# Performance work log

Measured on AMD Instinct MI355X. Metric: run time of the kernel, lower is better.

The kernel has to match this reference:

```python
import jax, jax.numpy as jnp
import numpy as np

N, E, G = 20000, 320000, 64   # nodes, edges, graphs in batch
DIN, DH, H, C = 128, 64, 8, 32  # in dim, hidden per head, heads, classes
NEG_SLOPE = 0.2


def setup_inputs() -> dict:
    key = jax.random.key(0)
    ks = jax.random.split(key, 20)
    s = lambda fan: 1.0 / np.sqrt(fan)
    inp = {
        "g_feats": jax.random.normal(ks[0], (N, DIN), jnp.float32),
        "src": jax.random.randint(ks[1], (E,), 0, N),
        "dst": jax.random.randint(ks[2], (E,), 0, N),
        "graph_ids": jnp.sort(jax.random.randint(ks[3], (N,), 0, G)),
        # input layer (linear): dim_in -> dim_h
        "W_in": jax.random.normal(ks[4], (DIN, DH), jnp.float32) * s(DIN),
        "b_in": jnp.zeros((DH,), jnp.float32),
        # GATv2 layer 1: dim_h -> H * dim_h
        "Wsrc1": jax.random.normal(ks[5], (DH, H * DH), jnp.float32) * s(DH),
        "bsrc1": jnp.zeros((H * DH,), jnp.float32),
        "Wdst1": jax.random.normal(ks[6], (DH, H * DH), jnp.float32) * s(DH),
        "bdst1": jnp.zeros((H * DH,), jnp.float32),
        "attn1": jax.random.normal(ks[7], (H, DH), jnp.float32) * s(DH),
        "bias1": jnp.zeros((H * DH,), jnp.float32),
        # GATv2 layer 2
        "Wsrc2": jax.random.normal(ks[8], (DH, H * DH), jnp.float32) * s(DH),
        "bsrc2": jnp.zeros((H * DH,), jnp.float32),
        "Wdst2": jax.random.normal(ks[9], (DH, H * DH), jnp.float32) * s(DH),
        "bdst2": jnp.zeros((H * DH,), jnp.float32),
        "attn2": jax.random.normal(ks[10], (H, DH), jnp.float32) * s(DH),
        "bias2": jnp.zeros((H * DH,), jnp.float32),
        # classification head: Linear(DH,DH) -> relu -> Linear(DH,C) -> softmax
        "Wh1": jax.random.normal(ks[11], (DH, DH), jnp.float32) * s(DH),
        "bh1": jnp.zeros((DH,), jnp.float32),
        "Wh2": jax.random.normal(ks[12], (DH, C), jnp.float32) * s(DH),
        "bh2": jnp.zeros((C,), jnp.float32),
    }
    return inp


def gatv2(h, src, dst, Ws, bs, Wd, bd, attn, bias):
    # DGL GATv2Conv: e_uv = attn . leaky_relu(fc_src(h_u) + fc_dst(h_v)),
    # softmax over incoming edges of v, aggregate fc_src(h_u).
    fs = (h @ Ws + bs).reshape(N, H, DH)
    fd = (h @ Wd + bd).reshape(N, H, DH)
    e = jax.nn.leaky_relu(fs[src] + fd[dst], NEG_SLOPE)      # [E, H, DH]
    scores = jnp.einsum('ehd,hd->eh', e, attn)               # [E, H]
    m = jax.ops.segment_max(scores, dst, num_segments=N)     # [N, H]
    m = jnp.where(jnp.isfinite(m), m, 0.0)                   # nodes w/o in-edges
    w = jnp.exp(scores - m[dst])
    denom = jax.ops.segment_sum(w, dst, num_segments=N)
    alpha = w / jnp.maximum(denom[dst], 1e-9)                # [E, H]
    out = jax.ops.segment_sum(fs[src] * alpha[:, :, None], dst, num_segments=N)
    return out + bias.reshape(1, H, DH)                      # [N, H, DH]


def reference(g_feats, src, dst, graph_ids, W_in, b_in,
              Wsrc1, bsrc1, Wdst1, bdst1, attn1, bias1,
              Wsrc2, bsrc2, Wdst2, bdst2, attn2, bias2,
              Wh1, bh1, Wh2, bh2):
    h = g_feats @ W_in + b_in                                # input layer ('linear')
    h = gatv2(h, src, dst, Wsrc1, bsrc1, Wdst1, bdst1, attn1, bias1).mean(axis=1)
    h = jax.nn.relu(h)
    h = gatv2(h, src, dst, Wsrc2, bsrc2, Wdst2, bdst2, attn2, bias2).mean(axis=1)
    # mean readout per graph
    sums = jax.ops.segment_sum(h, graph_ids, num_segments=G)
    counts = jax.ops.segment_sum(jnp.ones((N,), h.dtype), graph_ids, num_segments=G)
    hg = sums / jnp.maximum(counts, 1.0)[:, None]            # [G, DH]
    # head: Linear -> relu -> Linear -> softmax (dropout = identity at eval)
    logits = jax.nn.relu(hg @ Wh1 + bh1) @ Wh2 + bh2
    return jax.nn.softmax(logits, axis=-1)
```

## Files before the change

kernel.cpp:

```cpp
#include <hip/hip_runtime.h>

#define NN 20000
#define NE 320000
#define NG 64
#define DIN 128
#define DH 64
#define NH 8
#define HD 512
#define NC 32

typedef unsigned short ushort_t;
typedef unsigned int uint_t;

__device__ __forceinline__ ushort_t f2bf(float f) {
  uint_t x = __float_as_uint(f);
  uint_t r = (x + 0x7fffu + ((x >> 16) & 1u)) >> 16;
  return (ushort_t)r;
}

template<int PAT>
__device__ __forceinline__ float swz(float v) {
  return __int_as_float(__builtin_amdgcn_ds_swizzle(__float_as_int(v), PAT));
}

__device__ __forceinline__ void gemm_in_tile(const float* __restrict__ gf,
    const float* __restrict__ W_in, const float* __restrict__ b_in,
    float* __restrict__ h0, int tile) {
  __shared__ float AsIn[16][DIN];
  const int t = threadIdx.x;
  const int row0 = tile * 16;
  for (int i = t; i < 16 * DIN; i += 256)
    AsIn[i >> 7][i & 127] = gf[(size_t)(row0 + (i >> 7)) * DIN + (i & 127)];
  __syncthreads();
  const int c = t & 63, rg = t >> 6;
  float acc[4] = {0.f, 0.f, 0.f, 0.f};
  for (int k = 0; k < DIN; ++k) {
    float w = W_in[k * DH + c];
#pragma unroll
    for (int i = 0; i < 4; ++i) acc[i] += AsIn[rg * 4 + i][k] * w;
  }
  float b = b_in[c];
#pragma unroll
  for (int i = 0; i < 4; ++i)
    h0[(size_t)(row0 + rg * 4 + i) * DH + c] = acc[i] + b;
}

__device__ __forceinline__ void pair_tile(const float* __restrict__ A,
    const float* __restrict__ Ws, const float* __restrict__ bs,
    const float* __restrict__ Wd, const float* __restrict__ bd,
    ushort_t* __restrict__ fsb, float* __restrict__ fd, int tile) {
  __shared__ float AsP[16][DH];
  const int t = threadIdx.x;
  const bool isFd = tile >= (NN / 16);
  const int bx = isFd ? tile - (NN / 16) : tile;
  const float* W = isFd ? Wd : Ws;
  const float* b = isFd ? bd : bs;
  const int row0 = bx * 16;
  {
    int idx = t * 4;
    int r = idx >> 6, k = idx & 63;
    *(float4*)&AsP[r][k] = *(const float4*)&A[(size_t)(row0 + r) * DH + k];
  }
  __syncthreads();
  const int tc = t & 127;
  const int tr = t >> 7;
  float acc[8][4];
#pragma unroll
  for (int r = 0; r < 8; ++r)
#pragma unroll
    for (int c = 0; c < 4; ++c) acc[r][c] = 0.f;
#pragma unroll 4
  for (int k = 0; k < DH; ++k) {
    float4 wv = *(const float4*)&W[k * HD + 4 * tc];
#pragma unroll
    for (int r = 0; r < 8; ++r) {
      float a = AsP[tr * 8 + r][k];
      acc[r][0] += a * wv.x; acc[r][1] += a * wv.y;
      acc[r][2] += a * wv.z; acc[r][3] += a * wv.w;
    }
  }
  float4 bv = *(const float4*)&b[4 * tc];
#pragma unroll
  for (int r = 0; r < 8; ++r) {
    int row = row0 + tr * 8 + r;
    float v0 = acc[r][0] + bv.x, v1 = acc[r][1] + bv.y;
    float v2 = acc[r][2] + bv.z, v3 = acc[r][3] + bv.w;
    if (!isFd) {
      ushort4 o;
      o.x = f2bf(v0); o.y = f2bf(v1); o.z = f2bf(v2); o.w = f2bf(v3);
      *(ushort4*)&fsb[(size_t)row * HD + 4 * tc] = o;
    } else {
      *(float4*)&fd[(size_t)row * HD + 4 * tc] = make_float4(v0, v1, v2, v3);
    }
  }
}

__global__ __launch_bounds__(256) void k_pre(const float* __restrict__ gf,
    const float* __restrict__ W_in, const float* __restrict__ b_in,
    float* __restrict__ h0, const int* __restrict__ dst, int* __restrict__ counts,
    const int* __restrict__ gid, int* __restrict__ gs) {
  const int bid = blockIdx.x;
  if (bid < NN / 16) {
    gemm_in_tile(gf, W_in, b_in, h0, bid);
  } else if (bid < NN / 16 + NE / 256) {
    int e = (bid - NN / 16) * 256 + threadIdx.x;
    atomicAdd(&counts[dst[e]], 1);
  } else {
    int i = (bid - (NN / 16 + NE / 256)) * 256 + threadIdx.x;
    if (i > NN) return;
    if (i == 0) {
      for (int g = 0; g <= gid[0]; ++g) gs[g] = 0;
    } else if (i == NN) {
      for (int g = gid[NN - 1] + 1; g <= NG; ++g) gs[g] = NN;
    } else {
      int a = gid[i - 1], b2 = gid[i];
      for (int g = a + 1; g <= b2; ++g) gs[g] = i;
    }
  }
}

__global__ __launch_bounds__(256) void k_assign(const int* __restrict__ counts,
    int* __restrict__ row_beg, int* __restrict__ row_end, int* __restrict__ cursor,
    int* __restrict__ gcounter) {
  const int i = blockIdx.x * 256 + threadIdx.x;
  const int lane = threadIdx.x & 63;
  int cnt = (i < NN) ? counts[i] : 0;
  int pre = cnt;
#pragma unroll
  for (int d = 1; d < 64; d <<= 1) {
    int o = __shfl_up(pre, d);
    if (lane >= d) pre += o;
  }
  int total = __shfl(pre, 63);
  int excl = pre - cnt;
  int base = 0;
  if (lane == 63 && total > 0) base = atomicAdd(gcounter, total);
  base = __shfl(base, 63);
  if (i < NN) {
    int b = base + excl;
    row_beg[i] = b;
    row_end[i] = b + cnt;
    cursor[i] = b;
  }
}

__global__ __launch_bounds__(256) void k_scatpair(const float* __restrict__ A,
    const float* __restrict__ Ws, const float* __restrict__ bs,
    const float* __restrict__ Wd, const float* __restrict__ bd,
    ushort_t* __restrict__ fsb, float* __restrict__ fd,
    const int* __restrict__ dst, const int* __restrict__ src,
    int* __restrict__ cursor, int* __restrict__ src_sorted) {
  const int bid = blockIdx.x;
  if (bid < 2 * (NN / 16)) {
    pair_tile(A, Ws, bs, Wd, bd, fsb, fd, bid);
  } else {
    int e = (bid - 2 * (NN / 16)) * 256 + threadIdx.x;
    int p = atomicAdd(&cursor[dst[e]], 1);
    src_sorted[p] = src[e];
  }
}

__global__ __launch_bounds__(256) void k_pair(const float* __restrict__ A,
    const float* __restrict__ Ws, const float* __restrict__ bs,
    const float* __restrict__ Wd, const float* __restrict__ bd,
    ushort_t* __restrict__ fsb, float* __restrict__ fd) {
  pair_tile(A, Ws, bs, Wd, bd, fsb, fd, blockIdx.x);
}

__global__ __launch_bounds__(256) void k_gat(const ushort_t* __restrict__ fsb,
    const float* __restrict__ fd, const int* __restrict__ src_sorted,
    const int* __restrict__ row_beg, const int* __restrict__ row_end,
    const float* __restrict__ attn, const float* __restrict__ bias,
    float* __restrict__ hout, int do_relu) {
  const int lane = threadIdx.x & 63;
  const int v = blockIdx.x * 4 + (threadIdx.x >> 6);
  const int fi = lane * 8;
  float fdv[8], av[8];
  *(float4*)&fdv[0] = *(const float4*)&fd[(size_t)v * HD + fi];
  *(float4*)&fdv[4] = *(const float4*)&fd[(size_t)v * HD + fi + 4];
  *(float4*)&av[0]  = *(const float4*)&attn[fi];
  *(float4*)&av[4]  = *(const float4*)&attn[fi + 4];
  int e = row_beg[v];
  const int end = row_end[v];
  float m = -3.4e38f, sum = 0.f;
  float acc[8];
#pragma unroll
  for (int i = 0; i < 8; ++i) acc[i] = 0.f;
  for (; e + 1 < end; e += 2) {
    int sA = src_sorted[e], sB = src_sorted[e + 1];
    uint4 uA = *(const uint4*)&fsb[(size_t)sA * HD + fi];
    uint4 uB = *(const uint4*)&fsb[(size_t)sB * HD + fi];
    float fA[8], fB[8];
    fA[0] = __uint_as_float(uA.x << 16); fA[1] = __uint_as_float(uA.x & 0xffff0000u);
    fA[2] = __uint_as_float(uA.y << 16); fA[3] = __uint_as_float(uA.y & 0xffff0000u);
    fA[4] = __uint_as_float(uA.z << 16); fA[5] = __uint_as_float(uA.z & 0xffff0000u);
    fA[6] = __uint_as_float(uA.w << 16); fA[7] = __uint_as_float(uA.w & 0xffff0000u);
    fB[0] = __uint_as_float(uB.x << 16); fB[1] = __uint_as_float(uB.x & 0xffff0000u);
    fB[2] = __uint_as_float(uB.y << 16); fB[3] = __uint_as_float(uB.y & 0xffff0000u);
    fB[4] = __uint_as_float(uB.z << 16); fB[5] = __uint_as_float(uB.z & 0xffff0000u);
    fB[6] = __uint_as_float(uB.w << 16); fB[7] = __uint_as_float(uB.w & 0xffff0000u);
    float pA = 0.f, pB = 0.f;
#pragma unroll
    for (int i = 0; i < 8; ++i) {
      float xA = fA[i] + fdv[i];
      float lA = fmaxf(xA, 0.f) + 0.2f * fminf(xA, 0.f);
      pA = fmaf(av[i], lA, pA);
      float xB = fB[i] + fdv[i];
      float lB = fmaxf(xB, 0.f) + 0.2f * fminf(xB, 0.f);
      pB = fmaf(av[i], lB, pB);
    }
    pA += swz<0x041F>(pA); pB += swz<0x041F>(pB);
    pA += swz<0x081F>(pA); pB += swz<0x081F>(pB);
    pA += swz<0x101F>(pA); pB += swz<0x101F>(pB);
    float mn = fmaxf(m, fmaxf(pA, pB));
    float scale = __expf(m - mn);
    float wA = __expf(pA - mn), wB = __expf(pB - mn);
    sum = fmaf(sum, scale, wA + wB);
#pragma unroll
    for (int i = 0; i < 8; ++i)
      acc[i] = fmaf(acc[i], scale, fmaf(wA, fA[i], wB * fB[i]));
    m = mn;
  }
  if (e < end) {
    int sA = src_sorted[e];
    uint4 uA = *(const uint4*)&fsb[(size_t)sA * HD + fi];
    float fA[8];
    fA[0] = __uint_as_float(uA.x << 16); fA[1] = __uint_as_float(uA.x & 0xffff0000u);
    fA[2] = __uint_as_float(uA.y << 16); fA[3] = __uint_as_float(uA.y & 0xffff0000u);
    fA[4] = __uint_as_float(uA.z << 16); fA[5] = __uint_as_float(uA.z & 0xffff0000u);
    fA[6] = __uint_as_float(uA.w << 16); fA[7] = __uint_as_float(uA.w & 0xffff0000u);
    float pA = 0.f;
#pragma unroll
    for (int i = 0; i < 8; ++i) {
      float xA = fA[i] + fdv[i];
      float lA = fmaxf(xA, 0.f) + 0.2f * fminf(xA, 0.f);
      pA = fmaf(av[i], lA, pA);
    }
    pA += swz<0x041F>(pA);
    pA += swz<0x081F>(pA);
    pA += swz<0x101F>(pA);
    float mn = fmaxf(m, pA);
    float scale = __expf(m - mn);
    float wA = __expf(pA - mn);
    sum = fmaf(sum, scale, wA);
#pragma unroll
    for (int i = 0; i < 8; ++i)
      acc[i] = fmaf(acc[i], scale, wA * fA[i]);
  }
  float inv = 1.f / fmaxf(sum, 1e-9f);
  float outv[8];
#pragma unroll
  for (int i = 0; i < 8; ++i) outv[i] = fmaf(acc[i], inv, bias[fi + i]);
#pragma unroll
  for (int i = 0; i < 8; ++i) {
    outv[i] += swz<0x201F>(outv[i]);
    outv[i] += swz<0x401F>(outv[i]);
    outv[i] += __shfl_xor(outv[i], 32);
    outv[i] *= 0.125f;
    if (do_relu) outv[i] = fmaxf(outv[i], 0.f);
  }
  if (lane < 8) {
    *(float4*)&hout[(size_t)v * DH + lane * 8]     = make_float4(outv[0], outv[1], outv[2], outv[3]);
    *(float4*)&hout[(size_t)v * DH + lane * 8 + 4] = make_float4(outv[4], outv[5], outv[6], outv[7]);
  }
}

__global__ __launch_bounds__(256) void k_head(const float* __restrict__ h2,
    const int* __restrict__ gsv, const float* __restrict__ Wh1,
    const float* __restrict__ bh1, const float* __restrict__ Wh2,
    const float* __restrict__ bh2, float* __restrict__ out) {
  __shared__ float part[4][DH];
  __shared__ float hg[DH];
  __shared__ float hid[DH];
  __shared__ float logits[NC];
  const int g = blockIdx.x;
  const int t = threadIdx.x;
  const int f = t & 63, chunk = t >> 6;
  int start = gsv[g], stop = gsv[g + 1];
  float s = 0.f;
  for (int r = start + chunk; r < stop; r += 4) s += h2[(size_t)r * DH + f];
  part[chunk][f] = s;
  __syncthreads();
  if (t < DH) {
    float tot = part[0][t] + part[1][t] + part[2][t] + part[3][t];
    hg[t] = tot / fmaxf((float)(stop - start), 1.f);
  }
  __syncthreads();
  if (t < DH) {
    float a = 0.f;
    for (int k = 0; k < DH; ++k) a += hg[k] * Wh1[k * DH + t];
    hid[t] = fmaxf(a + bh1[t], 0.f);
  }
  __syncthreads();
  if (t < NC) {
    float l = 0.f;
    for (int k = 0; k < DH; ++k) l += hid[k] * Wh2[k * NC + t];
    logits[t] = l + bh2[t];
  }
  __syncthreads();
  if (t == 0) {
    float mx = logits[0];
    for (int i = 1; i < NC; ++i) mx = fmaxf(mx, logits[i]);
    float sm = 0.f;
    for (int i = 0; i < NC; ++i) {
      float wv = __expf(logits[i] - mx);
      logits[i] = wv;
      sm += wv;
    }
    float inv = 1.f / sm;
    for (int i = 0; i < NC; ++i) out[g * NC + i] = logits[i] * inv;
  }
}

extern "C" void kernel_launch(void* const* d_in, const int* in_sizes, int n_in,
                              void* d_out, int out_size, void* d_ws, size_t ws_size,
                              hipStream_t stream) {
  const float* g_feats = (const float*)d_in[0];
  const int*   src     = (const int*)d_in[1];
  const int*   dst     = (const int*)d_in[2];
  const int*   gid     = (const int*)d_in[3];
  const float* W_in    = (const float*)d_in[4];
  const float* b_in    = (const float*)d_in[5];
  const float* Wsrc1   = (const float*)d_in[6];
  const float* bsrc1   = (const float*)d_in[7];
  const float* Wdst1   = (const float*)d_in[8];
  const float* bdst1   = (const float*)d_in[9];
  const float* attn1   = (const float*)d_in[10];
  const float* bias1   = (const float*)d_in[11];
  const float* Wsrc2   = (const float*)d_in[12];
  const float* bsrc2   = (const float*)d_in[13];
  const float* Wdst2   = (const float*)d_in[14];
  const float* bdst2   = (const float*)d_in[15];
  const float* attn2   = (const float*)d_in[16];
  const float* bias2   = (const float*)d_in[17];
  const float* Wh1     = (const float*)d_in[18];
  const float* bh1     = (const float*)d_in[19];
  const float* Wh2     = (const float*)d_in[20];
  const float* bh2     = (const float*)d_in[21];

  char* ws = (char*)d_ws;
  size_t off = 0;
  auto A = [&](size_t bytes) -> char* {
    char* q = ws + off;
    off = (off + bytes + 255) & ~(size_t)255;
    return q;
  };
  float*    h0         = (float*)A((size_t)NN * DH * 4);
  float*    h1         = (float*)A((size_t)NN * DH * 4);
  float*    h2         = (float*)A((size_t)NN * DH * 4);
  ushort_t* fsb        = (ushort_t*)A((size_t)NN * HD * 2);
  float*    fd         = (float*)A((size_t)NN * HD * 4);
  int*      row_beg    = (int*)A((size_t)NN * 4);
  int*      row_end    = (int*)A((size_t)NN * 4);
  int*      cursor     = (int*)A((size_t)NN * 4);
  int*      src_sorted = (int*)A((size_t)NE * 4);
  int*      gs         = (int*)A((size_t)(NG + 1) * 4);
  int*      counts     = (int*)A((size_t)(NN + 1) * 4);

  const int nb16 = NN / 16;
  const int histb = NE / 256;
  const int gbb = (NN + 256) / 256;

  hipMemsetAsync(counts, 0, (size_t)(NN + 1) * 4, stream);

  k_pre<<<nb16 + histb + gbb, 256, 0, stream>>>(g_feats, W_in, b_in, h0,
                                                dst, counts, gid, gs);
  k_assign<<<(NN + 255) / 256, 256, 0, stream>>>(counts, row_beg, row_end,
                                                 cursor, &counts[NN]);
  k_scatpair<<<2 * nb16 + histb, 256, 0, stream>>>(h0, Wsrc1, bsrc1, Wdst1, bdst1,
                                                   fsb, fd, dst, src, cursor, src_sorted);
  k_gat<<<NN / 4, 256, 0, stream>>>(fsb, fd, src_sorted, row_beg, row_end,
                                    attn1, bias1, h1, 1);
  k_pair<<<2 * nb16, 256, 0, stream>>>(h1, Wsrc2, bsrc2, Wdst2, bdst2, fsb, fd);
  k_gat<<<NN / 4, 256, 0, stream>>>(fsb, fd, src_sorted, row_beg, row_end,
                                    attn2, bias2, h2, 0);
  k_head<<<NG, 256, 0, stream>>>(h2, gs, Wh1, bh1, Wh2, bh2, (float*)d_out);
}
```

Measured before the change: 341.8 us.

## Retile projection GEMM to 32 rows x 512 threads and unroll GAT edge loop by four

The fsrc/fdst projection now uses 512-thread blocks. Each thread owns one output column across 32 rows, replacing the previous 16-row tiles with a 4-column-per-thread layout. This halves the block count and reuses each weight load across more rows, but it writes bf16 outputs as scalar 2-byte stores. The GAT aggregation loop now processes four edges per iteration instead of two, exposing more independent gathers for memory-level parallelism at the cost of higher register pressure. The tail is now a loop and correctly updates the running max.

```diff
diff --git a/kernel.cpp b/kernel.cpp
--- a/kernel.cpp
+++ b/kernel.cpp
@@ -45,53 +45,48 @@
     h0[(size_t)(row0 + rg * 4 + i) * DH + c] = acc[i] + b;
 }
 
+#define ROWS_P 32
+#define TPM 625
 __device__ __forceinline__ void pair_tile(const float* __restrict__ A,
     const float* __restrict__ Ws, const float* __restrict__ bs,
     const float* __restrict__ Wd, const float* __restrict__ bd,
     ushort_t* __restrict__ fsb, float* __restrict__ fd, int tile) {
-  __shared__ float AsP[16][DH];
+  __shared__ float4 AsP4[ROWS_P][16];
   const int t = threadIdx.x;
-  const bool isFd = tile >= (NN / 16);
-  const int bx = isFd ? tile - (NN / 16) : tile;
+  const bool isFd = tile >= TPM;
+  const int bx = isFd ? tile - TPM : tile;
   const float* W = isFd ? Wd : Ws;
   const float* b = isFd ? bd : bs;
-  const int row0 = bx * 16;
+  const int row0 = bx * ROWS_P;
   {
-    int idx = t * 4;
-    int r = idx >> 6, k = idx & 63;
-    *(float4*)&AsP[r][k] = *(const float4*)&A[(size_t)(row0 + r) * DH + k];
-  }
-  __syncthreads();
-  const int tc = t & 127;
-  const int tr = t >> 7;
-  float acc[8][4];
-#pragma unroll
-  for (int r = 0; r < 8; ++r)
-#pragma unroll
-    for (int c = 0; c < 4; ++c) acc[r][c] = 0.f;
-#pragma unroll 4
-  for (int k = 0; k < DH; ++k) {
-    float4 wv = *(const float4*)&W[k * HD + 4 * tc];
-#pragma unroll
-    for (int r = 0; r < 8; ++r) {
-      float a = AsP[tr * 8 + r][k];
-      acc[r][0] += a * wv.x; acc[r][1] += a * wv.y;
-      acc[r][2] += a * wv.z; acc[r][3] += a * wv.w;
-    }
-  }
-  float4 bv = *(const float4*)&b[4 * tc];
-#pragma unroll
-  for (int r = 0; r < 8; ++r) {
-    int row = row0 + tr * 8 + r;
-    float v0 = acc[r][0] + bv.x, v1 = acc[r][1] + bv.y;
-    float v2 = acc[r][2] + bv.z, v3 = acc[r][3] + bv.w;
-    if (!isFd) {
-      ushort4 o;
-      o.x = f2bf(v0); o.y = f2bf(v1); o.z = f2bf(v2); o.w = f2bf(v3);
-      *(ushort4*)&fsb[(size_t)row * HD + 4 * tc] = o;
-    } else {
-      *(float4*)&fd[(size_t)row * HD + 4 * tc] = make_float4(v0, v1, v2, v3);
-    }
+    int row = t >> 4, kq = t & 15;
+    AsP4[row][kq] = *(const float4*)&A[(size_t)(row0 + row) * DH + 4 * kq];
+  }
+  __syncthreads();
+  const int c = t;
+  float acc[ROWS_P];
+#pragma unroll
+  for (int r = 0; r < ROWS_P; ++r) acc[r] = 0.f;
+  for (int kb = 0; kb < 16; ++kb) {
+    float w0 = W[(size_t)(4 * kb + 0) * HD + c];
+    float w1 = W[(size_t)(4 * kb + 1) * HD + c];
+    float w2 = W[(size_t)(4 * kb + 2) * HD + c];
+    float w3 = W[(size_t)(4 * kb + 3) * HD + c];
+#pragma unroll
+    for (int r = 0; r < ROWS_P; ++r) {
+      float4 a = AsP4[r][kb];
+      acc[r] = fmaf(a.x, w0, fmaf(a.y, w1, fmaf(a.z, w2, fmaf(a.w, w3, acc[r]))));
+    }
+  }
+  float bv = b[c];
+  if (!isFd) {
+#pragma unroll
+    for (int r = 0; r < ROWS_P; ++r)
+      fsb[(size_t)(row0 + r) * HD + c] = f2bf(acc[r] + bv);
+  } else {
+#pragma unroll
+    for (int r = 0; r < ROWS_P; ++r)
+      fd[(size_t)(row0 + r) * HD + c] = acc[r] + bv;
   }
 }
 
@@ -100,13 +95,14 @@
     float* __restrict__ h0, const int* __restrict__ dst, int* __restrict__ counts,
     const int* __restrict__ gid, int* __restrict__ gs) {
   const int bid = blockIdx.x;
-  if (bid < NN / 16) {
+  const int NB_IN = NN / 16;
+  if (bid < NB_IN) {
     gemm_in_tile(gf, W_in, b_in, h0, bid);
-  } else if (bid < NN / 16 + NE / 256) {
-    int e = (bid - NN / 16) * 256 + threadIdx.x;
+  } else if (bid < NB_IN + NE / 256) {
+    int e = (bid - NB_IN) * 256 + threadIdx.x;
     atomicAdd(&counts[dst[e]], 1);
   } else {
-    int i = (bid - (NN / 16 + NE / 256)) * 256 + threadIdx.x;
+    int i = (bid - (NB_IN + NE / 256)) * 256 + threadIdx.x;
     if (i > NN) return;
     if (i == 0) {
       for (int g = 0; g <= gid[0]; ++g) gs[g] = 0;
@@ -144,23 +140,23 @@
   }
 }
 
-__global__ __launch_bounds__(256) void k_scatpair(const float* __restrict__ A,
+__global__ __launch_bounds__(512) void k_scatpair(const float* __restrict__ A,
     const float* __restrict__ Ws, const float* __restrict__ bs,
     const float* __restrict__ Wd, const float* __restrict__ bd,
     ushort_t* __restrict__ fsb, float* __restrict__ fd,
     const int* __restrict__ dst, const int* __restrict__ src,
     int* __restrict__ cursor, int* __restrict__ src_sorted) {
   const int bid = blockIdx.x;
-  if (bid < 2 * (NN / 16)) {
+  if (bid < 2 * TPM) {
     pair_tile(A, Ws, bs, Wd, bd, fsb, fd, bid);
   } else {
-    int e = (bid - 2 * (NN / 16)) * 256 + threadIdx.x;
+    int e = (bid - 2 * TPM) * 512 + threadIdx.x;
     int p = atomicAdd(&cursor[dst[e]], 1);
     src_sorted[p] = src[e];
   }
 }
 
-__global__ __launch_bounds__(256) void k_pair(const float* __restrict__ A,
+__global__ __launch_bounds__(512) void k_pair(const float* __restrict__ A,
     const float* __restrict__ Ws, const float* __restrict__ bs,
     const float* __restrict__ Wd, const float* __restrict__ bd,
     ushort_t* __restrict__ fsb, float* __restrict__ fd) {
@@ -186,11 +182,14 @@
   float acc[8];
 #pragma unroll
   for (int i = 0; i < 8; ++i) acc[i] = 0.f;
-  for (; e + 1 < end; e += 2) {
-    int sA = src_sorted[e], sB = src_sorted[e + 1];
+  for (; e + 3 < end; e += 4) {
+    int sA = src_sorted[e],     sB = src_sorted[e + 1];
+    int sC = src_sorted[e + 2], sD = src_sorted[e + 3];
     uint4 uA = *(const uint4*)&fsb[(size_t)sA * HD + fi];
     uint4 uB = *(const uint4*)&fsb[(size_t)sB * HD + fi];
-    float fA[8], fB[8];
+    uint4 uC = *(const uint4*)&fsb[(size_t)sC * HD + fi];
+    uint4 uD = *(const uint4*)&fsb[(size_t)sD * HD + fi];
+    float fA[8], fB[8], fC[8], fD[8];
     fA[0] = __uint_as_float(uA.x << 16); fA[1] = __uint_as_float(uA.x & 0xffff0000u);
     fA[2] = __uint_as_float(uA.y << 16); fA[3] = __uint_as_float(uA.y & 0xffff0000u);
     fA[4] = __uint_as_float(uA.z << 16); fA[5] = __uint_as_float(uA.z & 0xffff0000u);
@@ -199,29 +198,41 @@
     fB[2] = __uint_as_float(uB.y << 16); fB[3] = __uint_as_float(uB.y & 0xffff0000u);
     fB[4] = __uint_as_float(uB.z << 16); fB[5] = __uint_as_float(uB.z & 0xffff0000u);
     fB[6] = __uint_as_float(uB.w << 16); fB[7] = __uint_as_float(uB.w & 0xffff0000u);
-    float pA = 0.f, pB = 0.f;
+    fC[0] = __uint_as_float(uC.x << 16); fC[1] = __uint_as_float(uC.x & 0xffff0000u);
+    fC[2] = __uint_as_float(uC.y << 16); fC[3] = __uint_as_float(uC.y & 0xffff0000u);
+    fC[4] = __uint_as_float(uC.z << 16); fC[5] = __uint_as_float(uC.z & 0xffff0000u);
+    fC[6] = __uint_as_float(uC.w << 16); fC[7] = __uint_as_float(uC.w & 0xffff0000u);
+    fD[0] = __uint_as_float(uD.x << 16); fD[1] = __uint_as_float(uD.x & 0xffff0000u);
+    fD[2] = __uint_as_float(uD.y << 16); fD[3] = __uint_as_float(uD.y & 0xffff0000u);
+    fD[4] = __uint_as_float(uD.z << 16); fD[5] = __uint_as_float(uD.z & 0xffff0000u);
+    fD[6] = __uint_as_float(uD.w << 16); fD[7] = __uint_as_float(uD.w & 0xffff0000u);
+    float pA = 0.f, pB = 0.f, pC = 0.f, pD = 0.f;
 #pragma unroll
     for (int i = 0; i < 8; ++i) {
       float xA = fA[i] + fdv[i];
-      float lA = fmaxf(xA, 0.f) + 0.2f * fminf(xA, 0.f);
-      pA = fmaf(av[i], lA, pA);
+      pA = fmaf(av[i], fmaxf(xA, 0.f) + 0.2f * fminf(xA, 0.f), pA);
       float xB = fB[i] + fdv[i];
-      float lB = fmaxf(xB, 0.f) + 0.2f * fminf(xB, 0.f);
-      pB = fmaf(av[i], lB, pB);
-    }
-    pA += swz<0x041F>(pA); pB += swz<0x041F>(pB);
-    pA += swz<0x081F>(pA); pB += swz<0x081F>(pB);
-    pA += swz<0x101F>(pA); pB += swz<0x101F>(pB);
-    float mn = fmaxf(m, fmaxf(pA, pB));
+      pB = fmaf(av[i], fmaxf(xB, 0.f) + 0.2f * fminf(xB, 0.f), pB);
+      float xC = fC[i] + fdv[i];
+      pC = fmaf(av[i], fmaxf(xC, 0.f) + 0.2f * fminf(xC, 0.f), pC);
+      float xD = fD[i] + fdv[i];
+      pD = fmaf(av[i], fmaxf(xD, 0.f) + 0.2f * fminf(xD, 0.f), pD);
+    }
+    pA += swz<0x041F>(pA); pB += swz<0x041F>(pB); pC += swz<0x041F>(pC); pD += swz<0x041F>(pD);
+    pA += swz<0x081F>(pA); pB += swz<0x081F>(pB); pC += swz<0x081F>(pC); pD += swz<0x081F>(pD);
+    pA += swz<0x101F>(pA); pB += swz<0x101F>(pB); pC += swz<0x101F>(pC); pD += swz<0x101F>(pD);
+    float mn = fmaxf(fmaxf(m, fmaxf(pA, pB)), fmaxf(pC, pD));
     float scale = __expf(m - mn);
     float wA = __expf(pA - mn), wB = __expf(pB - mn);
-    sum = fmaf(sum, scale, wA + wB);
+    float wC = __expf(pC - mn), wD = __expf(pD - mn);
+    sum = fmaf(sum, scale, (wA + wB) + (wC + wD));
 #pragma unroll
     for (int i = 0; i < 8; ++i)
-      acc[i] = fmaf(acc[i], scale, fmaf(wA, fA[i], wB * fB[i]));
+      acc[i] = fmaf(acc[i], scale,
+                    fmaf(wA, fA[i], fmaf(wB, fB[i], fmaf(wC, fC[i], wD * fD[i]))));
     m = mn;
   }
-  if (e < end) {
+  for (; e < end; ++e) {
     int sA = src_sorted[e];
     uint4 uA = *(const uint4*)&fsb[(size_t)sA * HD + fi];
     float fA[8];
@@ -233,8 +244,7 @@
 #pragma unroll
     for (int i = 0; i < 8; ++i) {
       float xA = fA[i] + fdv[i];
-      float lA = fmaxf(xA, 0.f) + 0.2f * fminf(xA, 0.f);
-      pA = fmaf(av[i], lA, pA);
+      pA = fmaf(av[i], fmaxf(xA, 0.f) + 0.2f * fminf(xA, 0.f), pA);
     }
     pA += swz<0x041F>(pA);
     pA += swz<0x081F>(pA);
@@ -246,6 +256,7 @@
 #pragma unroll
     for (int i = 0; i < 8; ++i)
       acc[i] = fmaf(acc[i], scale, wA * fA[i]);
+    m = mn;
   }
   float inv = 1.f / fmaxf(sum, 1e-9f);
   float outv[8];
@@ -357,21 +368,22 @@
   int*      gs         = (int*)A((size_t)(NG + 1) * 4);
   int*      counts     = (int*)A((size_t)(NN + 1) * 4);
 
-  const int nb16 = NN / 16;
+  const int NB_IN = NN / 16;
   const int histb = NE / 256;
   const int gbb = (NN + 256) / 256;
+  const int scatb = NE / 512;
 
   hipMemsetAsync(counts, 0, (size_t)(NN + 1) * 4, stream);
 
-  k_pre<<<nb16 + histb + gbb, 256, 0, stream>>>(g_feats, W_in, b_in, h0,
-                                                dst, counts, gid, gs);
+  k_pre<<<NB_IN + histb + gbb, 256, 0, stream>>>(g_feats, W_in, b_in, h0,
+                                                 dst, counts, gid, gs);
   k_assign<<<(NN + 255) / 256, 256, 0, stream>>>(counts, row_beg, row_end,
                                                  cursor, &counts[NN]);
-  k_scatpair<<<2 * nb16 + histb, 256, 0, stream>>>(h0, Wsrc1, bsrc1, Wdst1, bdst1,
-                                                   fsb, fd, dst, src, cursor, src_sorted);
+  k_scatpair<<<2 * TPM + scatb, 512, 0, stream>>>(h0, Wsrc1, bsrc1, Wdst1, bdst1,
+                                                  fsb, fd, dst, src, cursor, src_sorted);
   k_gat<<<NN / 4, 256, 0, stream>>>(fsb, fd, src_sorted, row_beg, row_end,
                                     attn1, bias1, h1, 1);
-  k_pair<<<2 * nb16, 256, 0, stream>>>(h1, Wsrc2, bsrc2, Wdst2, bdst2, fsb, fd);
+  k_pair<<<2 * TPM, 512, 0, stream>>>(h1, Wsrc2, bsrc2, Wdst2, bdst2, fsb, fd);
   k_gat<<<NN / 4, 256, 0, stream>>>(fsb, fd, src_sorted, row_beg, row_end,
                                     attn2, bias2, h2, 0);
   k_head<<<NG, 256, 0, stream>>>(h2, gs, Wh1, bh1, Wh2, bh2, (float*)d_out);
```

Measured after the change: 381.5 us. 1.12x slower.
